# Optimization experiments

Hardware: AMD Instinct MI355X
Metric: run time of the kernel (lower is better)

## Reference

```python
import jax, jax.numpy as jnp
import numpy as np

# ---- static dims (from init_kwargs / Hydra defaults) ----
B_, N_MESH, G, HEADS, DH = 2, 100000, 64, 8, 64
DIM = 256
D_MODEL = HEADS * DH              # 512
EXPAND, D_STATE, D_CONV = 2, 64, 3
D_INNER = EXPAND * D_MODEL        # 1024
HEADDIM = 64
NHEADS = D_INNER // HEADDIM       # 16
CONV_DIM = D_INNER + 2 * D_STATE  # 1152
D_IN_PROJ = 2 * D_INNER + 2 * D_STATE + 2 * NHEADS  # 2208


def _ssd_scan(x, dt, A, B, C):
    """Selective state-space scan (SSD / Mamba2 recurrence).
    x:(bb,L,H,P) dt:(bb,L,H) A:(H,) B,C:(bb,L,N). Returns y:(bb,L,H,P)."""
    bb, L, H, P = x.shape
    N = B.shape[-1]
    xs = jnp.moveaxis(x, 1, 0)   # (L,bb,H,P)
    dts = jnp.moveaxis(dt, 1, 0)  # (L,bb,H)
    Bs = jnp.moveaxis(B, 1, 0)   # (L,bb,N)
    Cs = jnp.moveaxis(C, 1, 0)
    h0 = jnp.zeros((bb, H, P, N), x.dtype)

    def step(h, inp):
        x_t, dt_t, B_t, C_t = inp
        dA = jnp.exp(dt_t * A)                                   # (bb,H)
        h = dA[..., None, None] * h + (dt_t[..., None] * x_t)[..., None] * B_t[:, None, None, :]
        y_t = jnp.einsum('bhpn,bn->bhp', h, C_t)
        return h, y_t

    _, ys = jax.lax.scan(step, h0, (xs, dts, Bs, Cs))
    return jnp.moveaxis(ys, 0, 1)


def _hydra(u, in_proj_w, conv_w, conv_b, dt_bias, A_log, fc_D_w, D, norm_w, out_proj_w):
    """Hydra (bidirectional Mamba2) forward, slow (non mem-eff) path."""
    b, L, _ = u.shape
    zxbcdt = u @ in_proj_w.T                                     # (b,L,2208)
    z = zxbcdt[..., :D_INNER]
    xBC = zxbcdt[..., D_INNER:D_INNER + CONV_DIM]
    dt_raw = zxbcdt[..., D_INNER + CONV_DIM:]                    # (b,L,2*NHEADS)
    # forward heads + time-flipped backward heads stacked along batch
    dt = jnp.concatenate([dt_raw[..., :NHEADS], jnp.flip(dt_raw[..., NHEADS:], axis=1)], axis=0)
    dt = jax.nn.softplus(dt + dt_bias)                           # (2b,L,NHEADS)
    # depthwise non-causal 'same' conv1d + SiLU
    xBC = jax.lax.conv_general_dilated(
        xBC.transpose(0, 2, 1), conv_w, (1,), [(1, 1)],
        dimension_numbers=('NCH', 'OIH', 'NCH'), feature_group_count=CONV_DIM)
    xBC = jax.nn.silu(xBC + conv_b[None, :, None]).transpose(0, 2, 1)
    x = xBC[..., :D_INNER]
    Bc = xBC[..., D_INNER:D_INNER + D_STATE]
    Cc = xBC[..., D_INNER + D_STATE:]
    x_og = x
    x2 = jnp.concatenate([x, jnp.flip(x, 1)], 0).reshape(2 * b, L, NHEADS, HEADDIM)
    B2 = jnp.concatenate([Bc, jnp.flip(Bc, 1)], 0)
    C2 = jnp.concatenate([Cc, jnp.flip(Cc, 1)], 0)
    A = -jnp.exp(A_log)                                          # (NHEADS,)
    y = _ssd_scan(x2, dt, A, B2, C2).reshape(2 * b, L, D_INNER)
    # shift by one (strictly off-diagonal parts), zero first position
    y = jnp.pad(y[:, :-1], ((0, 0), (1, 0), (0, 0)))
    diag = x_og @ fc_D_w.T + D                                   # (b,L,NHEADS)
    y = y[:b] + jnp.flip(y[b:], 1) + x_og * jnp.repeat(diag, HEADDIM, axis=-1)
    # gated RMSNorm
    y = y * jax.nn.silu(z)
    y = y * jax.lax.rsqrt(jnp.mean(y * y, axis=-1, keepdims=True) + 1e-5) * norm_w
    return y @ out_proj_w.T                                      # (b,L,D_MODEL)


def _forward(slice_token, slice_weights, in_proj_w, conv_w, conv_b, dt_bias, A_log,
             fc_D_w, D, norm_w, out_proj_w, to_out_w, to_out_b):
    b, h, g, c = slice_token.shape
    u = slice_token.transpose(0, 2, 1, 3).reshape(b, g, h * c)   # b g (h c)
    out = _hydra(u, in_proj_w, conv_w, conv_b, dt_bias, A_log, fc_D_w, D, norm_w, out_proj_w)
    ost = out.reshape(b, g, h, c).transpose(0, 2, 1, 3)          # b h g c
    out_x = jnp.einsum('bhgc,bhng->bhnc', ost, slice_weights)    # gather back to mesh points
    out_x = out_x.transpose(0, 2, 1, 3).reshape(b, out_x.shape[2], h * c)  # b n (h c)
    return out_x @ to_out_w.T + to_out_b


def setup_inputs() -> dict:
    key = jax.random.key(0)
    ks = jax.random.split(key, 14)
    f32 = jnp.float32
    inp = {}
    inp['slice_token'] = jax.random.normal(ks[0], (B_, HEADS, G, DH), f32)
    inp['slice_weights'] = jax.random.uniform(ks[1], (B_, HEADS, N_MESH, G), f32)
    inp['in_proj_w'] = jax.random.normal(ks[2], (D_IN_PROJ, D_MODEL), f32) * (D_MODEL ** -0.5)
    inp['conv_w'] = jax.random.normal(ks[3], (CONV_DIM, 1, D_CONV), f32) * 0.3
    inp['conv_b'] = jax.random.normal(ks[4], (CONV_DIM,), f32) * 0.02
    inp['dt_bias'] = jnp.log(jnp.expm1(jax.random.uniform(ks[5], (NHEADS,), f32, 0.001, 0.1)))
    inp['A_log'] = jnp.log(jax.random.uniform(ks[6], (NHEADS,), f32, 1.0, 8.0))
    inp['fc_D_w'] = jax.random.normal(ks[7], (NHEADS, D_INNER), f32) * (D_INNER ** -0.5)
    inp['D'] = jax.random.normal(ks[8], (NHEADS,), f32) * 0.1 + 1.0
    inp['norm_w'] = jnp.ones((D_INNER,), f32)
    inp['out_proj_w'] = jax.random.normal(ks[9], (D_MODEL, D_INNER), f32) * (D_INNER ** -0.5)
    inp['to_out_w'] = jax.random.normal(ks[10], (DIM, D_MODEL), f32) * (D_MODEL ** -0.5)
    inp['to_out_b'] = jnp.zeros((DIM,), f32)
    return inp


def reference(slice_token, slice_weights, in_proj_w, conv_w, conv_b, dt_bias, A_log,
              fc_D_w, D, norm_w, out_proj_w, to_out_w, to_out_b):
    return _forward(slice_token, slice_weights, in_proj_w, conv_w, conv_b, dt_bias,
                    A_log, fc_D_w, D, norm_w, out_proj_w, to_out_w, to_out_b)
```

## Files before the change

kernel.cpp:

```cpp
#include <hip/hip_runtime.h>
#include <hip/hip_bf16.h>
#include <math.h>

#define NB 2
#define LL 64
#define NMESH 100000
#define HEADS_O 8
#define DHC 64
#define DMODEL 512
#define DINNER 1024
#define DSTATE 64
#define NH 16
#define CONVDIM 1152
#define DINPROJ 2208
#define DOUT 256
#define NCHUNK 6250

typedef __attribute__((ext_vector_type(8))) short short8v;
typedef __attribute__((ext_vector_type(4))) float f32x4;

__device__ __forceinline__ unsigned short f2bf(float f) {
  union { float f; unsigned u; } v; v.f = f;
  unsigned u = v.u;
  u += 0x7FFFu + ((u >> 16) & 1u);
  return (unsigned short)(u >> 16);
}

__device__ __forceinline__ short8v pack_bf16(float4 lo, float4 hi) {
  short8v r;
  r[0] = (short)f2bf(lo.x); r[1] = (short)f2bf(lo.y);
  r[2] = (short)f2bf(lo.z); r[3] = (short)f2bf(lo.w);
  r[4] = (short)f2bf(hi.x); r[5] = (short)f2bf(hi.y);
  r[6] = (short)f2bf(hi.z); r[7] = (short)f2bf(hi.w);
  return r;
}

__device__ __forceinline__ float dot4(float4 a, const float* b) {
  return a.x*b[0] + a.y*b[1] + a.z*b[2] + a.w*b[3];
}

__device__ __forceinline__ float silu(float s) { return s / (1.f + expf(-s)); }

__global__ void k_inproj(const float* __restrict__ st, const float* __restrict__ w,
                         float* __restrict__ zx) {
  int oc = blockIdx.x;
  int blc = blockIdx.y;
  int t = threadIdx.x;
  __shared__ float u[8][DMODEL];
  for (int idx = t; idx < 8*DMODEL; idx += 256) {
    int r = idx >> 9, m = idx & 511;
    int bl = blc*8 + r; int b = bl >> 6, l = bl & 63;
    u[r][m] = st[((size_t)(b*HEADS_O + (m >> 6))*LL + l)*DHC + (m & 63)];
  }
  __syncthreads();
  int o = oc*256 + t;
  if (o < DINPROJ) {
    const float4* wr = (const float4*)(w + (size_t)o*DMODEL);
    float acc[8] = {0,0,0,0,0,0,0,0};
    for (int m4 = 0; m4 < DMODEL/4; ++m4) {
      float4 wv = wr[m4];
      #pragma unroll
      for (int r = 0; r < 8; ++r) acc[r] += dot4(wv, &u[r][m4*4]);
    }
    #pragma unroll
    for (int r = 0; r < 8; ++r)
      zx[(size_t)(blc*8 + r)*DINPROJ + o] = acc[r];
  }
}

__global__ void k_convdt(const float* __restrict__ zx, const float* __restrict__ cw,
                         const float* __restrict__ cb, const float* __restrict__ dtb,
                         float* __restrict__ conv_out, float* __restrict__ dtbuf) {
  if (blockIdx.x < 576) {
    int i = blockIdx.x*256 + threadIdx.x;
    int c = i % CONVDIM; int l = (i / CONVDIM) % LL; int b = i / (CONVDIM*LL);
    float s = cb[c];
    #pragma unroll
    for (int k = 0; k < 3; ++k) {
      int tt = l - 1 + k;
      if (tt >= 0 && tt < LL)
        s += cw[c*3 + k] * zx[(size_t)(b*LL + tt)*DINPROJ + DINNER + c];
    }
    conv_out[i] = silu(s);
  } else {
    int i = (blockIdx.x - 576)*256 + threadIdx.x;
    if (i < 4*LL*NH) {
      int h = i & 15, l = (i >> 4) & 63, s = i >> 10;
      float v;
      if (s < 2)
        v = zx[(size_t)(s*LL + l)*DINPROJ + (DINNER + CONVDIM) + h];
      else
        v = zx[(size_t)((s-2)*LL + (63-l))*DINPROJ + (DINNER + CONVDIM) + 16 + h];
      v += dtb[h];
      dtbuf[i] = (v > 20.f) ? v : log1pf(expf(v));
    }
  }
}

__global__ void k_scan(const float* __restrict__ conv_out, const float* __restrict__ dtbuf,
                       const float* __restrict__ A_log, float* __restrict__ ybuf) {
  int blk = blockIdx.x;
  int s = blk >> 4, hh = blk & 15;
  int b = s & 1;
  bool rev = (s >= 2);
  int t = threadIdx.x;
  int wv = t >> 6, lane = t & 63;
  __shared__ float Bs[64*68];
  __shared__ float Cs[64*68];
  __shared__ float Xs[64*64];
  __shared__ float dts[64];
  __shared__ float Dc[64];

  for (int id = t; id < 4096; id += 256) {
    int tt0 = id >> 6, n = id & 63;
    int tt = rev ? (63 - tt0) : tt0;
    size_t base = (size_t)(b*LL + tt) * CONVDIM;
    Xs[tt0*64 + n] = conv_out[base + hh*64 + n];
    Bs[tt0*68 + n] = conv_out[base + DINNER + n];
    Cs[tt0*68 + n] = conv_out[base + DINNER + DSTATE + n];
  }
  if (t < 64) dts[t] = dtbuf[(size_t)(s*LL + t)*NH + hh];
  __syncthreads();
  if (t < 64) {
    float v = dts[t];
    #pragma unroll
    for (int m = 1; m < 64; m <<= 1) {
      float o = __shfl_up(v, m, 64);
      if (lane >= m) v += o;
    }
    Dc[t] = v;
  }
  __syncthreads();
  float A = -expf(A_log[hh]);
  float g[16];
  #pragma unroll
  for (int i = 0; i < 16; ++i) {
    int tt = wv + 4*i;
    int ta = lane;
    float gv = 0.f;
    if (ta <= tt) {
      const float* Br = &Bs[ta*68];
      const float* Cr = &Cs[tt*68];
      float dot = 0.f;
      #pragma unroll
      for (int n4 = 0; n4 < 16; ++n4) {
        float4 bv = *(const float4*)&Br[n4*4];
        float4 cv = *(const float4*)&Cr[n4*4];
        dot += bv.x*cv.x + bv.y*cv.y + bv.z*cv.z + bv.w*cv.w;
      }
      gv = dot * expf(A * (Dc[tt] - Dc[ta])) * dts[ta];
    }
    g[i] = gv;
  }
  __syncthreads();
  #pragma unroll
  for (int i = 0; i < 16; ++i) Bs[(wv + 4*i)*64 + lane] = g[i];
  __syncthreads();
  for (int id = t; id < 4096; id += 256) {
    int tt = id >> 6, p = id & 63;
    float y = 0.f;
    for (int ta = 0; ta <= tt; ++ta) y += Bs[tt*64 + ta] * Xs[ta*64 + p];
    ybuf[(size_t)(s*LL + tt)*DINNER + hh*64 + p] = y;
  }
}

__global__ void k_norm(const float* __restrict__ conv_out, const float* __restrict__ zx,
                       const float* __restrict__ yb, const float* __restrict__ fcD,
                       const float* __restrict__ Dd, const float* __restrict__ nw,
                       float* __restrict__ ynorm) {
  int bl = blockIdx.x; int b = bl >> 6, l = bl & 63;
  int t = threadIdx.x;
  __shared__ float xog[DINNER];
  __shared__ float diag[NH];
  __shared__ float wsum[4];
  size_t base = (size_t)bl * CONVDIM;
  for (int c = t; c < DINNER; c += 256) xog[c] = conv_out[base + c];
  __syncthreads();
  {
    int hh = t >> 4, j = t & 15;
    const float* fr = fcD + (size_t)hh*DINNER;
    float acc = 0.f;
    for (int k = 0; k < 64; ++k) acc += xog[j + 16*k] * fr[j + 16*k];
    #pragma unroll
    for (int m = 8; m >= 1; m >>= 1) acc += __shfl_xor(acc, m, 64);
    if (j == 0) diag[hh] = acc + Dd[hh];
  }
  __syncthreads();
  float ss = 0.f;
  float y2v[4];
  #pragma unroll
  for (int i = 0; i < 4; ++i) {
    int c = t + 256*i;
    float yf = (l == 0)  ? 0.f : yb[(size_t)(b*LL + l - 1)*DINNER + c];
    float yw = (l == 63) ? 0.f : yb[(size_t)((2+b)*LL + 62 - l)*DINNER + c];
    float y1 = yf + yw + xog[c]*diag[c >> 6];
    float z = zx[(size_t)bl*DINPROJ + c];
    float y2 = y1 * silu(z);
    y2v[i] = y2;
    ss += y2*y2;
  }
  #pragma unroll
  for (int m = 32; m >= 1; m >>= 1) ss += __shfl_xor(ss, m, 64);
  if ((t & 63) == 0) wsum[t >> 6] = ss;
  __syncthreads();
  float tot = wsum[0] + wsum[1] + wsum[2] + wsum[3];
  float scale = rsqrtf(tot * (1.f/1024.f) + 1e-5f);
  #pragma unroll
  for (int i = 0; i < 4; ++i) {
    int c = t + 256*i;
    ynorm[(size_t)bl*DINNER + c] = y2v[i] * scale * nw[c];
  }
}

__global__ void k_oproj(const float* __restrict__ ynorm, const float* __restrict__ opw,
                        float* __restrict__ oh) {
  int oc = blockIdx.x;
  int blc = blockIdx.y;
  int t = threadIdx.x;
  __shared__ float yr[4][DINNER];
  for (int idx = t; idx < 4*DINNER; idx += 256) {
    int r = idx >> 10, k = idx & 1023;
    yr[r][k] = ynorm[(size_t)(blc*4 + r)*DINNER + k];
  }
  __syncthreads();
  int o = oc*256 + t;
  const float4* wr = (const float4*)(opw + (size_t)o*DINNER);
  float acc[4] = {0,0,0,0};
  for (int k4 = 0; k4 < DINNER/4; ++k4) {
    float4 wv = wr[k4];
    #pragma unroll
    for (int r = 0; r < 4; ++r) acc[r] += dot4(wv, &yr[r][k4*4]);
  }
  #pragma unroll
  for (int r = 0; r < 4; ++r)
    oh[(size_t)(blc*4 + r)*DMODEL + o] = acc[r];
}

__global__ void k_mfrag(const float* __restrict__ oh, const float* __restrict__ tow,
                        unsigned short* __restrict__ mfp) {
  int bgc = blockIdx.x;
  int dc  = blockIdx.y;
  int t = threadIdx.x;
  __shared__ float orow[8][DMODEL];
  for (int idx = t; idx < 8*DMODEL; idx += 256) {
    int r = idx >> 9, m = idx & 511;
    orow[r][m] = oh[(size_t)(bgc*8 + r)*DMODEL + m];
  }
  __syncthreads();
  #pragma unroll
  for (int ii = 0; ii < 2; ++ii) {
    int idx = t + 256*ii;
    int h = idx >> 6, dl = idx & 63;
    int d = dc*64 + dl;
    const float4* wr = (const float4*)(tow + (size_t)d*DMODEL + h*64);
    float acc[8] = {0,0,0,0,0,0,0,0};
    #pragma unroll
    for (int c4 = 0; c4 < 16; ++c4) {
      float4 wv = wr[c4];
      #pragma unroll
      for (int r = 0; r < 8; ++r) acc[r] += dot4(wv, &orow[r][h*64 + c4*4]);
    }
    #pragma unroll
    for (int r = 0; r < 8; ++r) {
      int bg = bgc*8 + r; int b = bg >> 6, g = bg & 63;
      int kk = g >> 5;
      int ln = (d & 15) | (((g & 31) >> 3) << 4);
      int j = g & 7;
      mfp[((((size_t)(b*HEADS_O + h)*2 + kk)*16 + (d >> 4))*64 + ln)*8 + j] = f2bf(acc[r]);
    }
  }
}

__global__ __launch_bounds__(512, 1) void k_out_gemm(const float* __restrict__ W,
                                                     const unsigned short* __restrict__ mf,
                                                     const float* __restrict__ tob,
                                                     float* __restrict__ out) {
  int bx = blockIdx.x;
  int b    = bx >> 7;
  int base = bx & 127;
  int tid = threadIdx.x;
  int wv = tid >> 6, lane = tid & 63;
  int r16 = lane & 15, kg = lane >> 4;

  __shared__ __align__(16) unsigned short lsA[2][16][512];

  short8v B0[16], B1[16];
  {
    const unsigned short* mfb = mf + (size_t)b*(16*16*512) + lane*8;
    #pragma unroll
    for (int ks = 0; ks < 16; ++ks) {
      B0[ks] = *(const short8v*)(mfb + ((size_t)ks*16 + 2*wv    )*512);
      B1[ks] = *(const short8v*)(mfb + ((size_t)ks*16 + 2*wv + 1)*512);
    }
  }
  float bias0 = tob[wv*32 + r16];
  float bias1 = tob[wv*32 + 16 + r16];

  const float* wbase = W + ((size_t)(b*HEADS_O + wv)*NMESH + r16)*64 + kg*8;

  float4 a0, a1, a2, a3;
  float4 b0, b1, b2, b3;

  #define ALOADS(cc, v0, v1, v2, v3) do { \
    const float* p0 = wbase + (size_t)(cc)*1024; \
    v0 = *(const float4*)p0;        v1 = *(const float4*)(p0 + 4); \
    v2 = *(const float4*)(p0 + 32); v3 = *(const float4*)(p0 + 36); \
  } while (0)
  #define AWR(pp, v0, v1, v2, v3) do { \
    *(short8v*)&lsA[pp][2*wv    ][lane*8] = pack_bf16(v0, v1); \
    *(short8v*)&lsA[pp][2*wv + 1][lane*8] = pack_bf16(v2, v3); \
  } while (0)
  #define MFMA_STORE(pp, cc) do { \
    f32x4 acc0 = (f32x4){0.f,0.f,0.f,0.f}; \
    f32x4 acc1 = (f32x4){0.f,0.f,0.f,0.f}; \
    _Pragma("unroll") \
    for (int ks = 0; ks < 16; ++ks) { \
      short8v af = *(const short8v*)&lsA[pp][ks][lane*8]; \
      acc0 = __builtin_amdgcn_mfma_f32_16x16x32_bf16(af, B0[ks], acc0, 0, 0, 0); \
      acc1 = __builtin_amdgcn_mfma_f32_16x16x32_bf16(af, B1[ks], acc1, 0, 0, 0); \
    } \
    int rb = (cc)*16 + kg*4; \
    int cg = wv*32 + r16; \
    _Pragma("unroll") \
    for (int r = 0; r < 4; ++r) { \
      out[((size_t)b*NMESH + rb + r)*DOUT + cg]      = acc0[r] + bias0; \
      out[((size_t)b*NMESH + rb + r)*DOUT + cg + 16] = acc1[r] + bias1; \
    } \
  } while (0)
  #define KBAR() do { \
    asm volatile("s_waitcnt lgkmcnt(0)" ::: "memory"); \
    __builtin_amdgcn_sched_barrier(0); \
    __builtin_amdgcn_s_barrier(); \
    __builtin_amdgcn_sched_barrier(0); \
  } while (0)

  ALOADS(base, a0, a1, a2, a3);
  AWR(0, a0, a1, a2, a3);
  ALOADS(base + 128, b0, b1, b2, b3);
  KBAR();

  int c = base;
  int p = 0;
  for (;;) {
    if (c + 256 < NCHUNK) ALOADS(c + 256, a0, a1, a2, a3);
    __builtin_amdgcn_sched_barrier(0);
    MFMA_STORE(p, c);
    if (c + 128 >= NCHUNK) break;
    __builtin_amdgcn_sched_barrier(0);
    AWR(p ^ 1, b0, b1, b2, b3);
    KBAR();
    p ^= 1; c += 128;
    if (c + 256 < NCHUNK) ALOADS(c + 256, b0, b1, b2, b3);
    __builtin_amdgcn_sched_barrier(0);
    MFMA_STORE(p, c);
    if (c + 128 >= NCHUNK) break;
    __builtin_amdgcn_sched_barrier(0);
    AWR(p ^ 1, a0, a1, a2, a3);
    KBAR();
    p ^= 1; c += 128;
  }
  #undef ALOADS
  #undef AWR
  #undef MFMA_STORE
  #undef KBAR
}

extern "C" void kernel_launch(void* const* d_in, const int* in_sizes, int n_in,
                              void* d_out, int out_size, void* d_ws, size_t ws_size,
                              hipStream_t stream) {
  (void)in_sizes; (void)n_in; (void)out_size; (void)ws_size;
  const float* st   = (const float*)d_in[0];
  const float* sw   = (const float*)d_in[1];
  const float* ipw  = (const float*)d_in[2];
  const float* cw   = (const float*)d_in[3];
  const float* cb   = (const float*)d_in[4];
  const float* dtb  = (const float*)d_in[5];
  const float* alog = (const float*)d_in[6];
  const float* fcD  = (const float*)d_in[7];
  const float* Dd   = (const float*)d_in[8];
  const float* nw   = (const float*)d_in[9];
  const float* opw  = (const float*)d_in[10];
  const float* tow  = (const float*)d_in[11];
  const float* tob  = (const float*)d_in[12];
  float* out = (float*)d_out;
  unsigned char* ws = (unsigned char*)d_ws;

  float* zx   = (float*)(ws + 0);
  float* conv = (float*)(ws + 1130496);
  float* dtp  = (float*)(ws + 1720320);
  float* yb   = (float*)(ws + 1736704);
  float* ynm  = (float*)(ws + 2785280);
  float* oh   = (float*)(ws + 3309568);
  unsigned short* mfr = (unsigned short*)(ws + 3571712);

  k_inproj  <<<dim3(9, 16), 256, 0, stream>>>(st, ipw, zx);
  k_convdt  <<<592, 256, 0, stream>>>(zx, cw, cb, dtb, conv, dtp);
  k_scan    <<<64,  256, 0, stream>>>(conv, dtp, alog, yb);
  k_norm    <<<128, 256, 0, stream>>>(conv, zx, yb, fcD, Dd, nw, ynm);
  k_oproj   <<<dim3(2, 32), 256, 0, stream>>>(ynm, opw, oh);
  k_mfrag   <<<dim3(16, 4), 256, 0, stream>>>(oh, tow, mfr);
  k_out_gemm<<<256, 512, 0, stream>>>(sw, mfr, tob, out);
}
```

Before: 241.8 us.

## Fuse conv1d and softplus dt into scan and norm kernels, vectorize y accumulation

```diff
diff --git a/kernel.cpp b/kernel.cpp
--- a/kernel.cpp
+++ b/kernel.cpp
@@ -68,58 +68,52 @@
   }
 }
 
-__global__ void k_convdt(const float* __restrict__ zx, const float* __restrict__ cw,
-                         const float* __restrict__ cb, const float* __restrict__ dtb,
-                         float* __restrict__ conv_out, float* __restrict__ dtbuf) {
-  if (blockIdx.x < 576) {
-    int i = blockIdx.x*256 + threadIdx.x;
-    int c = i % CONVDIM; int l = (i / CONVDIM) % LL; int b = i / (CONVDIM*LL);
-    float s = cb[c];
-    #pragma unroll
-    for (int k = 0; k < 3; ++k) {
-      int tt = l - 1 + k;
-      if (tt >= 0 && tt < LL)
-        s += cw[c*3 + k] * zx[(size_t)(b*LL + tt)*DINPROJ + DINNER + c];
-    }
-    conv_out[i] = silu(s);
-  } else {
-    int i = (blockIdx.x - 576)*256 + threadIdx.x;
-    if (i < 4*LL*NH) {
-      int h = i & 15, l = (i >> 4) & 63, s = i >> 10;
-      float v;
-      if (s < 2)
-        v = zx[(size_t)(s*LL + l)*DINPROJ + (DINNER + CONVDIM) + h];
-      else
-        v = zx[(size_t)((s-2)*LL + (63-l))*DINPROJ + (DINNER + CONVDIM) + 16 + h];
-      v += dtb[h];
-      dtbuf[i] = (v > 20.f) ? v : log1pf(expf(v));
-    }
-  }
-}
-
-__global__ void k_scan(const float* __restrict__ conv_out, const float* __restrict__ dtbuf,
-                       const float* __restrict__ A_log, float* __restrict__ ybuf) {
+__global__ void k_scanF(const float* __restrict__ zx, const float* __restrict__ cw,
+                        const float* __restrict__ cb, const float* __restrict__ dtb,
+                        const float* __restrict__ A_log, float* __restrict__ ybuf) {
   int blk = blockIdx.x;
   int s = blk >> 4, hh = blk & 15;
   int b = s & 1;
   bool rev = (s >= 2);
   int t = threadIdx.x;
   int wv = t >> 6, lane = t & 63;
+  __shared__ float zr[64][192];
   __shared__ float Bs[64*68];
   __shared__ float Cs[64*68];
   __shared__ float Xs[64*64];
   __shared__ float dts[64];
   __shared__ float Dc[64];
 
+  for (int idx = t; idx < 64*192; idx += 256) {
+    int l = idx / 192, j = idx % 192;
+    int c = (j < 64) ? (hh*64 + j) : ((j < 128) ? (1024 + j - 64) : (1088 + j - 128));
+    zr[l][j] = zx[(size_t)(b*LL + l)*DINPROJ + DINNER + c];
+  }
+  if (t < 64) {
+    int tt = rev ? (63 - t) : t;
+    int ch = rev ? (16 + hh) : hh;
+    float v = zx[(size_t)(b*LL + tt)*DINPROJ + (DINNER + CONVDIM) + ch] + dtb[hh];
+    dts[t] = (v > 20.f) ? v : log1pf(expf(v));
+  }
+  __syncthreads();
   for (int id = t; id < 4096; id += 256) {
     int tt0 = id >> 6, n = id & 63;
     int tt = rev ? (63 - tt0) : tt0;
-    size_t base = (size_t)(b*LL + tt) * CONVDIM;
-    Xs[tt0*64 + n] = conv_out[base + hh*64 + n];
-    Bs[tt0*68 + n] = conv_out[base + DINNER + n];
-    Cs[tt0*68 + n] = conv_out[base + DINNER + DSTATE + n];
-  }
-  if (t < 64) dts[t] = dtbuf[(size_t)(s*LL + t)*NH + hh];
+    int cx = hh*64 + n, cB = 1024 + n, cC = 1088 + n;
+    float sx = cb[cx], sb = cb[cB], sc = cb[cC];
+    #pragma unroll
+    for (int k = 0; k < 3; ++k) {
+      int l = tt - 1 + k;
+      if (l >= 0 && l < 64) {
+        sx += cw[cx*3 + k] * zr[l][n];
+        sb += cw[cB*3 + k] * zr[l][64 + n];
+        sc += cw[cC*3 + k] * zr[l][128 + n];
+      }
+    }
+    Xs[tt0*64 + n] = silu(sx);
+    Bs[tt0*68 + n] = silu(sb);
+    Cs[tt0*68 + n] = silu(sc);
+  }
   __syncthreads();
   if (t < 64) {
     float v = dts[t];
@@ -154,27 +148,42 @@
   }
   __syncthreads();
   #pragma unroll
-  for (int i = 0; i < 16; ++i) Bs[(wv + 4*i)*64 + lane] = g[i];
-  __syncthreads();
-  for (int id = t; id < 4096; id += 256) {
-    int tt = id >> 6, p = id & 63;
-    float y = 0.f;
-    for (int ta = 0; ta <= tt; ++ta) y += Bs[tt*64 + ta] * Xs[ta*64 + p];
-    ybuf[(size_t)(s*LL + tt)*DINNER + hh*64 + p] = y;
-  }
-}
-
-__global__ void k_norm(const float* __restrict__ conv_out, const float* __restrict__ zx,
-                       const float* __restrict__ yb, const float* __restrict__ fcD,
-                       const float* __restrict__ Dd, const float* __restrict__ nw,
-                       float* __restrict__ ynorm) {
+  for (int i = 0; i < 16; ++i) Bs[(wv + 4*i)*68 + lane] = g[i];
+  __syncthreads();
+  for (int id = t; id < 1024; id += 256) {
+    int tt = id >> 4, p4 = (id & 15) * 4;
+    float4 y = {0.f, 0.f, 0.f, 0.f};
+    for (int ta = 0; ta <= tt; ++ta) {
+      float gv = Bs[tt*68 + ta];
+      float4 x = *(const float4*)&Xs[ta*64 + p4];
+      y.x += gv*x.x; y.y += gv*x.y; y.z += gv*x.z; y.w += gv*x.w;
+    }
+    *(float4*)&ybuf[(size_t)(s*LL + tt)*DINNER + hh*64 + p4] = y;
+  }
+}
+
+__global__ void k_norm(const float* __restrict__ zx, const float* __restrict__ cw,
+                       const float* __restrict__ cb, const float* __restrict__ yb,
+                       const float* __restrict__ fcD, const float* __restrict__ Dd,
+                       const float* __restrict__ nw, float* __restrict__ ynorm) {
   int bl = blockIdx.x; int b = bl >> 6, l = bl & 63;
   int t = threadIdx.x;
+  __shared__ float zs[3][DINNER];
   __shared__ float xog[DINNER];
   __shared__ float diag[NH];
   __shared__ float wsum[4];
-  size_t base = (size_t)bl * CONVDIM;
-  for (int c = t; c < DINNER; c += 256) xog[c] = conv_out[base + c];
+  for (int idx = t; idx < 3*DINNER; idx += 256) {
+    int r = idx >> 10, c = idx & 1023;
+    int ll = l - 1 + r;
+    zs[r][c] = (ll >= 0 && ll < LL) ? zx[(size_t)(b*LL + ll)*DINPROJ + DINNER + c] : 0.f;
+  }
+  __syncthreads();
+  #pragma unroll
+  for (int i = 0; i < 4; ++i) {
+    int c = t + 256*i;
+    float s = cb[c] + cw[c*3]*zs[0][c] + cw[c*3+1]*zs[1][c] + cw[c*3+2]*zs[2][c];
+    xog[c] = silu(s);
+  }
   __syncthreads();
   {
     int hh = t >> 4, j = t & 15;
@@ -386,17 +395,14 @@
   unsigned char* ws = (unsigned char*)d_ws;
 
   float* zx   = (float*)(ws + 0);
-  float* conv = (float*)(ws + 1130496);
-  float* dtp  = (float*)(ws + 1720320);
-  float* yb   = (float*)(ws + 1736704);
-  float* ynm  = (float*)(ws + 2785280);
-  float* oh   = (float*)(ws + 3309568);
-  unsigned short* mfr = (unsigned short*)(ws + 3571712);
+  float* yb   = (float*)(ws + 1130496);
+  float* ynm  = (float*)(ws + 2179072);
+  float* oh   = (float*)(ws + 2703360);
+  unsigned short* mfr = (unsigned short*)(ws + 2965504);
 
   k_inproj  <<<dim3(9, 16), 256, 0, stream>>>(st, ipw, zx);
-  k_convdt  <<<592, 256, 0, stream>>>(zx, cw, cb, dtb, conv, dtp);
-  k_scan    <<<64,  256, 0, stream>>>(conv, dtp, alog, yb);
-  k_norm    <<<128, 256, 0, stream>>>(conv, zx, yb, fcD, Dd, nw, ynm);
+  k_scanF   <<<64,  256, 0, stream>>>(zx, cw, cb, dtb, alog, yb);
+  k_norm    <<<128, 256, 0, stream>>>(zx, cw, cb, yb, fcD, Dd, nw, ynm);
   k_oproj   <<<dim3(2, 32), 256, 0, stream>>>(ynm, opw, oh);
   k_mfrag   <<<dim3(16, 4), 256, 0, stream>>>(oh, tow, mfr);
   k_out_gemm<<<256, 512, 0, stream>>>(sw, mfr, tob, out);
```

New measurement: 248.0 us. 1.03x slower.

## Fuse norm, out-proj and to_out fragment kernels; deepen out-GEMM prefetch to two chunks

Applied to the files above, without the earlier changes.

```diff
diff --git a/kernel.cpp b/kernel.cpp
--- a/kernel.cpp
+++ b/kernel.cpp
@@ -164,36 +164,49 @@
   }
 }
 
-__global__ void k_norm(const float* __restrict__ conv_out, const float* __restrict__ zx,
-                       const float* __restrict__ yb, const float* __restrict__ fcD,
-                       const float* __restrict__ Dd, const float* __restrict__ nw,
-                       float* __restrict__ ynorm) {
-  int bl = blockIdx.x; int b = bl >> 6, l = bl & 63;
+__global__ __launch_bounds__(1024) void k_tail(const float* __restrict__ conv_out,
+                                               const float* __restrict__ zx,
+                                               const float* __restrict__ yb,
+                                               const float* __restrict__ fcD,
+                                               const float* __restrict__ Dd,
+                                               const float* __restrict__ nw,
+                                               const float* __restrict__ opw,
+                                               const float* __restrict__ tow,
+                                               unsigned short* __restrict__ mfp) {
+  int bl0 = blockIdx.x * 4;
   int t = threadIdx.x;
-  __shared__ float xog[DINNER];
-  __shared__ float diag[NH];
-  __shared__ float wsum[4];
-  size_t base = (size_t)bl * CONVDIM;
-  for (int c = t; c < DINNER; c += 256) xog[c] = conv_out[base + c];
+  int row = t >> 8, tl = t & 255;
+  int bl = bl0 + row; int b = bl >> 6, l = bl & 63;
+  __shared__ float xog[4][DINNER];
+  __shared__ float yrow[4][DINNER];
+  __shared__ float ohs[4][DMODEL];
+  __shared__ float diag[4][NH];
+  __shared__ float wsum[4][4];
+
+  #pragma unroll
+  for (int i = 0; i < 4; ++i) {
+    int c = tl + 256*i;
+    xog[row][c] = conv_out[(size_t)bl*CONVDIM + c];
+  }
   __syncthreads();
   {
-    int hh = t >> 4, j = t & 15;
+    int hh = tl >> 4, j = tl & 15;
     const float* fr = fcD + (size_t)hh*DINNER;
     float acc = 0.f;
-    for (int k = 0; k < 64; ++k) acc += xog[j + 16*k] * fr[j + 16*k];
+    for (int k = 0; k < 64; ++k) acc += xog[row][j + 16*k] * fr[j + 16*k];
     #pragma unroll
     for (int m = 8; m >= 1; m >>= 1) acc += __shfl_xor(acc, m, 64);
-    if (j == 0) diag[hh] = acc + Dd[hh];
+    if (j == 0) diag[row][hh] = acc + Dd[hh];
   }
   __syncthreads();
   float ss = 0.f;
   float y2v[4];
   #pragma unroll
   for (int i = 0; i < 4; ++i) {
-    int c = t + 256*i;
+    int c = tl + 256*i;
     float yf = (l == 0)  ? 0.f : yb[(size_t)(b*LL + l - 1)*DINNER + c];
     float yw = (l == 63) ? 0.f : yb[(size_t)((2+b)*LL + 62 - l)*DINNER + c];
-    float y1 = yf + yw + xog[c]*diag[c >> 6];
+    float y1 = yf + yw + xog[row][c]*diag[row][c >> 6];
     float z = zx[(size_t)bl*DINPROJ + c];
     float y2 = y1 * silu(z);
     y2v[i] = y2;
@@ -201,73 +214,44 @@
   }
   #pragma unroll
   for (int m = 32; m >= 1; m >>= 1) ss += __shfl_xor(ss, m, 64);
-  if ((t & 63) == 0) wsum[t >> 6] = ss;
-  __syncthreads();
-  float tot = wsum[0] + wsum[1] + wsum[2] + wsum[3];
+  if ((tl & 63) == 0) wsum[row][tl >> 6] = ss;
+  __syncthreads();
+  float tot = wsum[row][0] + wsum[row][1] + wsum[row][2] + wsum[row][3];
   float scale = rsqrtf(tot * (1.f/1024.f) + 1e-5f);
   #pragma unroll
   for (int i = 0; i < 4; ++i) {
-    int c = t + 256*i;
-    ynorm[(size_t)bl*DINNER + c] = y2v[i] * scale * nw[c];
-  }
-}
-
-__global__ void k_oproj(const float* __restrict__ ynorm, const float* __restrict__ opw,
-                        float* __restrict__ oh) {
-  int oc = blockIdx.x;
-  int blc = blockIdx.y;
-  int t = threadIdx.x;
-  __shared__ float yr[4][DINNER];
-  for (int idx = t; idx < 4*DINNER; idx += 256) {
-    int r = idx >> 10, k = idx & 1023;
-    yr[r][k] = ynorm[(size_t)(blc*4 + r)*DINNER + k];
-  }
-  __syncthreads();
-  int o = oc*256 + t;
-  const float4* wr = (const float4*)(opw + (size_t)o*DINNER);
-  float acc[4] = {0,0,0,0};
-  for (int k4 = 0; k4 < DINNER/4; ++k4) {
-    float4 wv = wr[k4];
-    #pragma unroll
-    for (int r = 0; r < 4; ++r) acc[r] += dot4(wv, &yr[r][k4*4]);
-  }
-  #pragma unroll
-  for (int r = 0; r < 4; ++r)
-    oh[(size_t)(blc*4 + r)*DMODEL + o] = acc[r];
-}
-
-__global__ void k_mfrag(const float* __restrict__ oh, const float* __restrict__ tow,
-                        unsigned short* __restrict__ mfp) {
-  int bgc = blockIdx.x;
-  int dc  = blockIdx.y;
-  int t = threadIdx.x;
-  __shared__ float orow[8][DMODEL];
-  for (int idx = t; idx < 8*DMODEL; idx += 256) {
-    int r = idx >> 9, m = idx & 511;
-    orow[r][m] = oh[(size_t)(bgc*8 + r)*DMODEL + m];
-  }
-  __syncthreads();
-  #pragma unroll
-  for (int ii = 0; ii < 2; ++ii) {
-    int idx = t + 256*ii;
-    int h = idx >> 6, dl = idx & 63;
-    int d = dc*64 + dl;
+    int c = tl + 256*i;
+    yrow[row][c] = y2v[i] * scale * nw[c];
+  }
+  __syncthreads();
+  if (t < 512) {
+    const float4* wr = (const float4*)(opw + (size_t)t*DINNER);
+    float acc[4] = {0,0,0,0};
+    for (int k4 = 0; k4 < DINNER/4; ++k4) {
+      float4 wv = wr[k4];
+      #pragma unroll
+      for (int r = 0; r < 4; ++r) acc[r] += dot4(wv, &yrow[r][k4*4]);
+    }
+    #pragma unroll
+    for (int r = 0; r < 4; ++r) ohs[r][t] = acc[r];
+  }
+  __syncthreads();
+  #pragma unroll
+  for (int ii = 0; ii < 8; ++ii) {
+    int idx = t + 1024*ii;
+    int r = idx >> 11;
+    int h = (idx >> 8) & 7;
+    int d = idx & 255;
     const float4* wr = (const float4*)(tow + (size_t)d*DMODEL + h*64);
-    float acc[8] = {0,0,0,0,0,0,0,0};
-    #pragma unroll
-    for (int c4 = 0; c4 < 16; ++c4) {
-      float4 wv = wr[c4];
-      #pragma unroll
-      for (int r = 0; r < 8; ++r) acc[r] += dot4(wv, &orow[r][h*64 + c4*4]);
-    }
-    #pragma unroll
-    for (int r = 0; r < 8; ++r) {
-      int bg = bgc*8 + r; int b = bg >> 6, g = bg & 63;
-      int kk = g >> 5;
-      int ln = (d & 15) | (((g & 31) >> 3) << 4);
-      int j = g & 7;
-      mfp[((((size_t)(b*HEADS_O + h)*2 + kk)*16 + (d >> 4))*64 + ln)*8 + j] = f2bf(acc[r]);
-    }
+    const float* op = &ohs[r][h*64];
+    float acc = 0.f;
+    #pragma unroll
+    for (int c4 = 0; c4 < 16; ++c4) acc += dot4(wr[c4], &op[c4*4]);
+    int blr = bl0 + r; int br = blr >> 6, g = blr & 63;
+    int kk = g >> 5;
+    int ln = (d & 15) | (((g & 31) >> 3) << 4);
+    int j = g & 7;
+    mfp[((((size_t)(br*HEADS_O + h)*2 + kk)*16 + (d >> 4))*64 + ln)*8 + j] = f2bf(acc);
   }
 }
 
@@ -282,7 +266,7 @@
   int wv = tid >> 6, lane = tid & 63;
   int r16 = lane & 15, kg = lane >> 4;
 
-  __shared__ __align__(16) unsigned short lsA[2][16][512];
+  __shared__ __align__(16) unsigned short lsA[2][2][16][512];
 
   short8v B0[16], B1[16];
   {
@@ -306,16 +290,16 @@
     v0 = *(const float4*)p0;        v1 = *(const float4*)(p0 + 4); \
     v2 = *(const float4*)(p0 + 32); v3 = *(const float4*)(p0 + 36); \
   } while (0)
-  #define AWR(pp, v0, v1, v2, v3) do { \
-    *(short8v*)&lsA[pp][2*wv    ][lane*8] = pack_bf16(v0, v1); \
-    *(short8v*)&lsA[pp][2*wv + 1][lane*8] = pack_bf16(v2, v3); \
+  #define AWR(pp, sl, v0, v1, v2, v3) do { \
+    *(short8v*)&lsA[pp][sl][2*wv    ][lane*8] = pack_bf16(v0, v1); \
+    *(short8v*)&lsA[pp][sl][2*wv + 1][lane*8] = pack_bf16(v2, v3); \
   } while (0)
-  #define MFMA_STORE(pp, cc) do { \
+  #define MFMA_STORE(pp, sl, cc) do { \
     f32x4 acc0 = (f32x4){0.f,0.f,0.f,0.f}; \
     f32x4 acc1 = (f32x4){0.f,0.f,0.f,0.f}; \
     _Pragma("unroll") \
     for (int ks = 0; ks < 16; ++ks) { \
-      short8v af = *(const short8v*)&lsA[pp][ks][lane*8]; \
+      short8v af = *(const short8v*)&lsA[pp][sl][ks][lane*8]; \
       acc0 = __builtin_amdgcn_mfma_f32_16x16x32_bf16(af, B0[ks], acc0, 0, 0, 0); \
       acc1 = __builtin_amdgcn_mfma_f32_16x16x32_bf16(af, B1[ks], acc1, 0, 0, 0); \
     } \
@@ -335,29 +319,29 @@
   } while (0)
 
   ALOADS(base, a0, a1, a2, a3);
-  AWR(0, a0, a1, a2, a3);
+  AWR(0, 0, a0, a1, a2, a3);
   ALOADS(base + 128, b0, b1, b2, b3);
+  AWR(0, 1, b0, b1, b2, b3);
   KBAR();
 
   int c = base;
   int p = 0;
   for (;;) {
-    if (c + 256 < NCHUNK) ALOADS(c + 256, a0, a1, a2, a3);
+    int cn = c + 256;
+    bool more = (cn < NCHUNK);
+    if (more) {
+      ALOADS(cn, a0, a1, a2, a3);
+      if (cn + 128 < NCHUNK) ALOADS(cn + 128, b0, b1, b2, b3);
+    }
     __builtin_amdgcn_sched_barrier(0);
-    MFMA_STORE(p, c);
-    if (c + 128 >= NCHUNK) break;
+    MFMA_STORE(p, 0, c);
+    if (c + 128 < NCHUNK) MFMA_STORE(p, 1, c + 128);
+    if (!more) break;
     __builtin_amdgcn_sched_barrier(0);
-    AWR(p ^ 1, b0, b1, b2, b3);
+    AWR(p ^ 1, 0, a0, a1, a2, a3);
+    if (cn + 128 < NCHUNK) AWR(p ^ 1, 1, b0, b1, b2, b3);
     KBAR();
-    p ^= 1; c += 128;
-    if (c + 256 < NCHUNK) ALOADS(c + 256, b0, b1, b2, b3);
-    __builtin_amdgcn_sched_barrier(0);
-    MFMA_STORE(p, c);
-    if (c + 128 >= NCHUNK) break;
-    __builtin_amdgcn_sched_barrier(0);
-    AWR(p ^ 1, a0, a1, a2, a3);
-    KBAR();
-    p ^= 1; c += 128;
+    p ^= 1; c = cn;
   }
   #undef ALOADS
   #undef AWR
@@ -389,15 +373,11 @@
   float* conv = (float*)(ws + 1130496);
   float* dtp  = (float*)(ws + 1720320);
   float* yb   = (float*)(ws + 1736704);
-  float* ynm  = (float*)(ws + 2785280);
-  float* oh   = (float*)(ws + 3309568);
-  unsigned short* mfr = (unsigned short*)(ws + 3571712);
+  unsigned short* mfr = (unsigned short*)(ws + 2785280);
 
   k_inproj  <<<dim3(9, 16), 256, 0, stream>>>(st, ipw, zx);
   k_convdt  <<<592, 256, 0, stream>>>(zx, cw, cb, dtb, conv, dtp);
   k_scan    <<<64,  256, 0, stream>>>(conv, dtp, alog, yb);
-  k_norm    <<<128, 256, 0, stream>>>(conv, zx, yb, fcD, Dd, nw, ynm);
-  k_oproj   <<<dim3(2, 32), 256, 0, stream>>>(ynm, opw, oh);
-  k_mfrag   <<<dim3(16, 4), 256, 0, stream>>>(oh, tow, mfr);
+  k_tail    <<<32, 1024, 0, stream>>>(conv, zx, yb, fcD, Dd, nw, opw, tow, mfr);
   k_out_gemm<<<256, 512, 0, stream>>>(sw, mfr, tob, out);
 }
```

Measured after the change: 380.5 us. 1.57x slower.
